# Optimization experiments

Measured on AMD Instinct MI355X. Metric: run time of the kernel, lower is better.

The kernel has to match this reference:

```python
import jax, jax.numpy as jnp
import numpy as np

N_NODES = 50000
N_EDGES = 800000
GEN_EPS = 1e-7
LN_EPS = 1e-5


def _mlp3_tanh(x, w0, b0, w1, b1, w2, b2):
    x = jnp.tanh(x @ w0.T + b0)
    x = jnp.tanh(x @ w1.T + b1)
    return jnp.tanh(x @ w2.T + b2)


def _gen_conv(x, src, dst, edge_attr, w0, b0, ln_w, ln_b, w1, b1):
    # GENConv(aggr='softmax', t=1): msg = relu(x_j + e) + eps
    msg = jax.nn.relu(x[src] + edge_attr) + GEN_EPS          # [E, 64]
    m = jax.ops.segment_max(msg, dst, num_segments=N_NODES)  # [N, 64]
    ex = jnp.exp(msg - m[dst])
    den = jax.ops.segment_sum(ex, dst, num_segments=N_NODES)
    alpha = ex / den[dst]                                    # scatter-softmax per dst
    agg = jax.ops.segment_sum(alpha * msg, dst, num_segments=N_NODES)
    h = x + agg                                              # x_r + aggregated messages
    # internal MLP: Linear(64->128), LayerNorm(128), ReLU, Linear(128->64)
    h = h @ w0.T + b0
    mu = jnp.mean(h, axis=-1, keepdims=True)
    var = jnp.mean((h - mu) ** 2, axis=-1, keepdims=True)
    h = ln_w * (h - mu) * jax.lax.rsqrt(var + LN_EPS) + ln_b
    h = jax.nn.relu(h)
    return h @ w1.T + b1


def setup_inputs() -> dict:
    key = jax.random.key(0)
    ks = jax.random.split(key, 32)
    s = 0.05
    d = {
        'node_features': jax.random.normal(ks[0], (N_NODES, 11), jnp.float32),
        'edge_features': jax.random.normal(ks[1], (N_EDGES, 3), jnp.float32),
        'edge_index': jax.random.randint(ks[2], (2, N_EDGES), 0, N_NODES, jnp.int32),
        'ne_w0': jax.random.normal(ks[3], (64, 11)) * s, 'ne_b0': jnp.zeros((64,)),
        'ne_w1': jax.random.normal(ks[4], (64, 64)) * s, 'ne_b1': jnp.zeros((64,)),
        'ne_w2': jax.random.normal(ks[5], (64, 64)) * s, 'ne_b2': jnp.zeros((64,)),
        'ee_w0': jax.random.normal(ks[6], (64, 3)) * s, 'ee_b0': jnp.zeros((64,)),
        'ee_w1': jax.random.normal(ks[7], (64, 64)) * s, 'ee_b1': jnp.zeros((64,)),
        'ee_w2': jax.random.normal(ks[8], (64, 64)) * s, 'ee_b2': jnp.zeros((64,)),
        'mp_w0': jax.random.normal(ks[9], (3, 128, 64)) * s,
        'mp_b0': jnp.zeros((3, 128)),
        'mp_ln_w': jnp.ones((3, 128)), 'mp_ln_b': jnp.zeros((3, 128)),
        'mp_w1': jax.random.normal(ks[10], (3, 64, 128)) * s,
        'mp_b1': jnp.zeros((3, 64)),
        'pi_w0': jax.random.normal(ks[11], (64, 64)) * s, 'pi_b0': jnp.zeros((64,)),
        'pi_w1': jax.random.normal(ks[12], (64, 64)) * s, 'pi_b1': jnp.zeros((64,)),
        'pi_w2': jax.random.normal(ks[13], (2, 64)) * s, 'pi_b2': jnp.zeros((2,)),
    }
    return {k: (v.astype(jnp.float32) if v.dtype != jnp.int32 else v) for k, v in d.items()}


def reference(node_features, edge_features, edge_index,
              ne_w0, ne_b0, ne_w1, ne_b1, ne_w2, ne_b2,
              ee_w0, ee_b0, ee_w1, ee_b1, ee_w2, ee_b2,
              mp_w0, mp_b0, mp_ln_w, mp_ln_b, mp_w1, mp_b1,
              pi_w0, pi_b0, pi_w1, pi_b1, pi_w2, pi_b2):
    src, dst = edge_index[0], edge_index[1]
    x = _mlp3_tanh(node_features, ne_w0, ne_b0, ne_w1, ne_b1, ne_w2, ne_b2)
    e = _mlp3_tanh(edge_features, ee_w0, ee_b0, ee_w1, ee_b1, ee_w2, ee_b2)
    for i in range(3):
        x = _gen_conv(x, src, dst, e, mp_w0[i], mp_b0[i], mp_ln_w[i], mp_ln_b[i], mp_w1[i], mp_b1[i])
    h = jnp.tanh(x @ pi_w0.T + pi_b0)
    h = jnp.tanh(h @ pi_w1.T + pi_b1)
    out = h @ pi_w2.T + pi_b2                 # [N, 2]
    # output.t().reshape(-1)[:n_turbines] == first column of out
    means = -30.0 + (out[:, 0] + 1.0) * 60.0 / 2.0
    return means
```

## Files before the change

kernel.cpp:

```cpp
#include <hip/hip_runtime.h>
#include <stdint.h>

#define N_NODES 50000
#define N_EDGES 800000

typedef unsigned short u16;
typedef unsigned int u32;
typedef __attribute__((ext_vector_type(8))) short short8;
typedef __attribute__((ext_vector_type(4))) float f32x4;
typedef __attribute__((ext_vector_type(4))) u32 u32x4;
typedef __attribute__((ext_vector_type(2))) u32 u32x2;

#define WAVE_SYNC() asm volatile("s_waitcnt lgkmcnt(0)" ::: "memory")

__device__ __forceinline__ float b2f(u16 v) {
    u32 u = ((u32)v) << 16; float f; __builtin_memcpy(&f, &u, 4); return f;
}
__device__ __forceinline__ u16 f2b(float f) {
    u32 u; __builtin_memcpy(&u, &f, 4);
    return (u16)((u + 0x8000u) >> 16);
}
__device__ __forceinline__ float lo2f(u32 p) {
    u32 u = p << 16; float f; __builtin_memcpy(&f, &u, 4); return f;
}
__device__ __forceinline__ float hi2f(u32 p) {
    u32 u = p & 0xffff0000u; float f; __builtin_memcpy(&f, &u, 4); return f;
}
__device__ __forceinline__ u32 pack2(float a, float b) {
    u32 ua, ub; __builtin_memcpy(&ua, &a, 4); __builtin_memcpy(&ub, &b, 4);
    return __builtin_amdgcn_perm(ub + 0x8000u, ua + 0x8000u, 0x07060302u);
}
__device__ __forceinline__ f32x4 mfma16(short8 a, short8 b, f32x4 c) {
    return __builtin_amdgcn_mfma_f32_16x16x32_bf16(a, b, c, 0, 0, 0);
}

#define TANH_TBL_N 192
__device__ __forceinline__ void build_tanh_tbl(float2* tbl) {
    int i = (int)threadIdx.x;
    if (i < TANH_TBL_N) {
        float x0 = i * 0.03125f, x1 = x0 + 0.03125f;
        float t0 = tanhf(x0), t1 = tanhf(x1);
        float s = (t1 - t0) * 32.f;
        tbl[i] = make_float2(fmaf(-s, x0, t0), s);
    }
    __syncthreads();
}
__device__ __forceinline__ float lut_tanh(const float2* __restrict__ tbl, float x) {
    float a = __builtin_fabsf(x);
    a = fminf(a, 5.96875f);
    int i = (int)(a * 32.f);
    float2 bs = tbl[i];
    float y = fmaf(bs.y, a, bs.x);
    u32 uy, ux; __builtin_memcpy(&uy, &y, 4); __builtin_memcpy(&ux, &x, 4);
    u32 r = (uy & 0x7fffffffu) | (ux & 0x80000000u);
    float o; __builtin_memcpy(&o, &r, 4); return o;
}

enum : int {
    NE_T0 = 0,     NE_B0 = 704,   NE_T1 = 768,   NE_B1 = 4864,  NE_T2 = 4928,  NE_B2 = 9024,
    EE_T0 = 9088,  EE_B0 = 9280,  EE_T1 = 9344,  EE_B1 = 13440, EE_T2 = 13504, EE_B2 = 17600,
    MP_T0 = 17664, MP_B0 = 42240, LNW_O = 42624, LNB_O = 43008, MP_T1 = 43392, MP_B1 = 67968,
    PI_T0 = 68160, PI_B0 = 72256, PI_T1 = 72320, PI_B1 = 76416, PI_W2 = 76480, PI_B2 = 76608,
    W_TOTAL = 76610
};

enum : int {
    FR_EE1 = 0, FR_EE2 = 4, FR_EE3 = 12, FR_NE1 = 20, FR_NE2 = 24, FR_NE3 = 32,
    FR_MP0 = 40, FR_MP1 = 88, FR_PI0 = 136, FR_PI1 = 144, FR_TOTAL = 152
};

#define OFF_W       ((size_t)0)
#define OFF_FLAG    ((size_t)0x60000)
#define OFF_WB      ((size_t)0x61000)
#define OFF_X0      ((size_t)0x90000)
#define OFF_X1      ((size_t)0x00D00000)
#define OFF_H64B    ((size_t)0x01A00000)
#define OFF_XB0     ((size_t)0x02080000)
#define OFF_E       ((size_t)0x02700000)
#define OFF_ROWPTR  ((size_t)0x08900000)
#define OFF_CURSOR  ((size_t)0x08940000)
#define OFF_PERM    ((size_t)0x08980000)
#define OFF_SRCS    ((size_t)0x08D00000)
#define OFF_BSUM    ((size_t)0x09080000)
#define OFF_XB1     ((size_t)0x09100000)

struct Ptrs24 { const void* p[24]; };


__global__ void detect_kernel(const void* nf, int* flag) {
    u32 w = ((const u32*)nf)[threadIdx.x & 63];
    u32 lo = w & 0xffffu;
    int e = (int)((lo >> 7) & 0xff);
    int good = ((e >= 118 && e <= 132) || lo == 0) ? 1 : 0;
    unsigned long long b = __ballot(good != 0);
    if (threadIdx.x == 0) *flag = (__popcll(b) >= 48) ? 1 : 0;
}

__global__ void convert_weights(Ptrs24 ps, float* __restrict__ W, const int* flag) {
    const int segIN[24] = {11,64,64,64,64,64, 3,64,64,64,64,64, 64,384,384,384,128,192, 64,64,64,64,128,2};
    const int segOUT[24]= {64, 1,64, 1,64, 1, 64, 1,64, 1,64, 1, 128, 1,  1,  1, 64,  1, 64, 1,64, 1,  1,1};
    const int segS[24]  = { 1, 1, 1, 1, 1, 1,  1, 1, 1, 1, 1, 1,   3, 1,  1,  1,  3,  1,  1, 1, 1, 1,  1,1};
    const int segTR[24] = { 1, 0, 1, 0, 1, 0,  1, 0, 1, 0, 1, 0,   1, 0,  0,  0,  1,  0,  1, 0, 1, 0,  0,0};
    int t = blockIdx.x * blockDim.x + threadIdx.x;
    if (t >= W_TOTAL) return;
    bool bf = (*flag != 0);
    int seg = 0, off = t;
    for (;;) {
        int cnt = segIN[seg] * segOUT[seg] * segS[seg];
        if (off < cnt) break;
        off -= cnt; seg++;
    }
    int srcIdx;
    if (segTR[seg]) {
        int per = segIN[seg] * segOUT[seg];
        int s = off / per, d = off % per;
        int j = d / segOUT[seg], i = d % segOUT[seg];
        srcIdx = s * per + i * segIN[seg] + j;
    } else {
        srcIdx = off;
    }
    const void* p = ps.p[seg];
    W[t] = bf ? b2f(((const u16*)p)[srcIdx]) : ((const float*)p)[srcIdx];
}

__global__ void make_frags(const float* __restrict__ W, u16* __restrict__ Wb) {
    const int base[15] = {FR_EE1,FR_EE2,FR_EE3,FR_NE1,FR_NE2,FR_NE3,
                          FR_MP0,FR_MP0+16,FR_MP0+32, FR_MP1,FR_MP1+16,FR_MP1+32,
                          FR_PI0,FR_PI1,FR_TOTAL};
    const int woff[14] = {EE_T0,EE_T1,EE_T2, NE_T0,NE_T1,NE_T2,
                          MP_T0,MP_T0+8192,MP_T0+16384, MP_T1,MP_T1+8192,MP_T1+16384,
                          PI_T0,PI_T1};
    const int kreal[14] = {3,64,64, 11,64,64, 64,64,64, 128,128,128, 64,64};
    const int nn[14]    = {64,64,64, 64,64,64, 128,128,128, 64,64,64, 64,64};
    int t = blockIdx.x * blockDim.x + threadIdx.x;
    if (t >= FR_TOTAL * 512) return;
    int f = t >> 9, r = t & 511, lane = r >> 3, j = r & 7;
    int l = 0;
    while (f >= base[l + 1]) l++;
    int lf = f - base[l];
    int NT = nn[l] >> 4;
    int kt = lf / NT, nt = lf % NT;
    int k = kt * 32 + (lane >> 4) * 8 + j;
    int n = nt * 16 + (lane & 15);
    float v = (k < kreal[l]) ? W[woff[l] + k * nn[l] + n] : 0.f;
    u32 u; __builtin_memcpy(&u, &v, 4);
    Wb[t] = (u16)((u + 0x7fffu + ((u >> 16) & 1u)) >> 16);
}


__global__ void hist_kernel(const int* __restrict__ dst, int* __restrict__ rowptr) {
    int e = blockIdx.x * blockDim.x + threadIdx.x;
    if (e < N_EDGES) atomicAdd(&rowptr[dst[e] + 1], 1);
}

__global__ void scanA(int* __restrict__ rowptr, int* __restrict__ bsum) {
    __shared__ int wsum[16];
    int tid = threadIdx.x, lane = tid & 63, wid = tid >> 6;
    int i0 = blockIdx.x * 2048 + tid * 2;
    int v0 = (i0 <= N_NODES) ? rowptr[i0] : 0;
    int v1 = (i0 + 1 <= N_NODES) ? rowptr[i0 + 1] : 0;
    int v = v0 + v1;
#pragma unroll
    for (int off = 1; off < 64; off <<= 1) {
        int t = __shfl_up(v, off, 64);
        if (lane >= off) v += t;
    }
    if (lane == 63) wsum[wid] = v;
    __syncthreads();
    if (tid == 0) { int a = 0; for (int w = 0; w < 16; w++) { a += wsum[w]; wsum[w] = a; } }
    __syncthreads();
    int incl = v + (wid ? wsum[wid - 1] : 0);
    if (i0 <= N_NODES) rowptr[i0] = incl - v1;
    if (i0 + 1 <= N_NODES) rowptr[i0 + 1] = incl;
    if (tid == 1023) bsum[blockIdx.x] = incl;
}
__global__ void scanB(int* __restrict__ bsum, int nb) {
    int lane = threadIdx.x;
    int v = (lane < nb) ? bsum[lane] : 0;
#pragma unroll
    for (int off = 1; off < 64; off <<= 1) {
        int t = __shfl_up(v, off, 64);
        if (lane >= off) v += t;
    }
    if (lane < nb) bsum[lane] = v;
}
__global__ void scanC(const int* __restrict__ bsum, int* __restrict__ rowptr,
                      int* __restrict__ cursor) {
    int i = blockIdx.x * 1024 + threadIdx.x;
    if (i > N_NODES) return;
    int b = i >> 11;
    int v = rowptr[i] + (b ? bsum[b - 1] : 0);
    rowptr[i] = v;
    if (i < N_NODES) cursor[i] = v;
}

__global__ void scatter_kernel(const int* __restrict__ dst, const int* __restrict__ src,
                               int* __restrict__ cursor, int* __restrict__ perm,
                               int* __restrict__ srcs) {
    int e = blockIdx.x * blockDim.x + threadIdx.x;
    if (e >= N_EDGES) return;
    int p = atomicAdd(&cursor[dst[e]], 1);
    perm[e] = p;
    srcs[p] = src[e];
}


template<int KT, int NT, int INSTR>
__device__ __forceinline__ void mfma_layer(const u32* ldsin, int lane,
        const short8* __restrict__ Wf, int basef, const float* __restrict__ bias, f32x4* acc) {
    int q = lane >> 4, mr = lane & 15;
#pragma unroll
    for (int nt = 0; nt < NT; nt++) acc[nt] = *(const f32x4*)(bias + nt * 16 + q * 4);
#pragma unroll
    for (int kt = 0; kt < KT; kt++) {
        short8 act = *(const short8*)(ldsin + mr * INSTR + kt * 16 + q * 4);
#pragma unroll
        for (int nt = 0; nt < NT; nt++)
            acc[nt] = mfma16(Wf[(basef + kt * NT + nt) * 64 + lane], act, acc[nt]);
    }
}

template<int KT, int NT>
__device__ __forceinline__ void mfma_layer_reg(const short8* act, int lane,
        const short8* __restrict__ Wf, int basef, const float* __restrict__ bias, f32x4* acc) {
    int q = lane >> 4;
#pragma unroll
    for (int nt = 0; nt < NT; nt++) acc[nt] = *(const f32x4*)(bias + nt * 16 + q * 4);
#pragma unroll
    for (int kt = 0; kt < KT; kt++)
#pragma unroll
        for (int nt = 0; nt < NT; nt++)
            acc[nt] = mfma16(Wf[(basef + kt * NT + nt) * 64 + lane], act[kt], acc[nt]);
}

template<int NT, int OUTSTR>
__device__ __forceinline__ void tanh_pack_lds(const f32x4* acc, u32* ldsout, int lane,
                                              const float2* __restrict__ tbl) {
    int q = lane >> 4, mr = lane & 15;
#pragma unroll
    for (int nt = 0; nt < NT; nt++) {
        f32x4 a = acc[nt];
        ldsout[mr * OUTSTR + nt * 8 + q * 2 + 0] = pack2(lut_tanh(tbl, a[0]), lut_tanh(tbl, a[1]));
        ldsout[mr * OUTSTR + nt * 8 + q * 2 + 1] = pack2(lut_tanh(tbl, a[2]), lut_tanh(tbl, a[3]));
    }
}


__global__ __launch_bounds__(256) void edge_encoder(const void* ef, u32* __restrict__ ebuf,
        const int* __restrict__ perm, const float* __restrict__ W,
        const short8* __restrict__ Wf, const int* flag) {
    __shared__ u32 lds[4 * 1152];
    __shared__ float2 tbl[TANH_TBL_N];
    build_tanh_tbl(tbl);
    int wv = threadIdx.x >> 6, lane = threadIdx.x & 63;
    u32* B0 = lds + wv * 1152;
    u32* B1 = B0 + 576;
    long ebase = (long)blockIdx.x * 64 + wv * 16;
    bool bf = (*flag != 0);
    if (lane < 16) {
        long e = ebase + lane;
        float i0, i1, i2;
        if (bf) { const u16* p = (const u16*)ef + e * 3; i0 = b2f(p[0]); i1 = b2f(p[1]); i2 = b2f(p[2]); }
        else    { const float* p = (const float*)ef + e * 3; i0 = p[0]; i1 = p[1]; i2 = p[2]; }
        u32* row = B0 + lane * 36;
        row[0] = pack2(i0, i1); row[1] = pack2(i2, 0.f);
#pragma unroll
        for (int d = 2; d < 16; d++) row[d] = 0;
    }
    WAVE_SYNC();
    f32x4 acc[4];
    mfma_layer<1, 4, 36>(B0, lane, Wf, FR_EE1, W + EE_B0, acc);
    tanh_pack_lds<4, 36>(acc, B1, lane, tbl);
    WAVE_SYNC();
    mfma_layer<2, 4, 36>(B1, lane, Wf, FR_EE2, W + EE_B1, acc);
    tanh_pack_lds<4, 36>(acc, B0, lane, tbl);
    WAVE_SYNC();
    mfma_layer<2, 4, 36>(B0, lane, Wf, FR_EE3, W + EE_B2, acc);
    tanh_pack_lds<4, 36>(acc, B1, lane, tbl);
    WAVE_SYNC();
    int ro = lane >> 2, cc = (lane & 3) * 8;
    long e = ebase + ro;
    long prow = perm[e];
    u32x4 v0 = *(const u32x4*)&B1[ro * 36 + cc];
    u32x4 v1 = *(const u32x4*)&B1[ro * 36 + cc + 4];
    *(u32x4*)&ebuf[prow * 32 + cc] = v0;
    *(u32x4*)&ebuf[prow * 32 + cc + 4] = v1;
}

__global__ __launch_bounds__(256) void node_encoder(const void* nf, float* __restrict__ x,
        u16* __restrict__ xbf, const float* __restrict__ W,
        const short8* __restrict__ Wf, const int* flag) {
    __shared__ u32 lds[4 * 1152];
    __shared__ float2 tbl[TANH_TBL_N];
    build_tanh_tbl(tbl);
    int wv = threadIdx.x >> 6, lane = threadIdx.x & 63;
    int q = lane >> 4, mr = lane & 15;
    u32* B0 = lds + wv * 1152;
    u32* B1 = B0 + 576;
    long nbase = (long)blockIdx.x * 64 + wv * 16;
    bool bf = (*flag != 0);
    if (lane < 16) {
        long n = nbase + lane;
        float in[12];
#pragma unroll
        for (int j = 0; j < 12; j++) in[j] = 0.f;
        if (n < N_NODES) {
#pragma unroll
            for (int j = 0; j < 11; j++)
                in[j] = bf ? b2f(((const u16*)nf)[n * 11 + j]) : ((const float*)nf)[n * 11 + j];
        }
        u32* row = B0 + lane * 36;
#pragma unroll
        for (int d = 0; d < 6; d++) row[d] = pack2(in[2 * d], in[2 * d + 1]);
#pragma unroll
        for (int d = 6; d < 16; d++) row[d] = 0;
    }
    WAVE_SYNC();
    f32x4 acc[4];
    mfma_layer<1, 4, 36>(B0, lane, Wf, FR_NE1, W + NE_B0, acc);
    tanh_pack_lds<4, 36>(acc, B1, lane, tbl);
    WAVE_SYNC();
    mfma_layer<2, 4, 36>(B1, lane, Wf, FR_NE2, W + NE_B1, acc);
    tanh_pack_lds<4, 36>(acc, B0, lane, tbl);
    WAVE_SYNC();
    mfma_layer<2, 4, 36>(B0, lane, Wf, FR_NE3, W + NE_B2, acc);
    long n = nbase + mr;
    if (n < N_NODES) {
#pragma unroll
        for (int nt = 0; nt < 4; nt++) {
            f32x4 v;
#pragma unroll
            for (int rr = 0; rr < 4; rr++) v[rr] = lut_tanh(tbl, acc[nt][rr]);
            *(f32x4*)(x + n * 64 + nt * 16 + q * 4) = v;
            u32x2 pb; pb.x = pack2(v[0], v[1]); pb.y = pack2(v[2], v[3]);
            *(u32x2*)&xbf[n * 64 + nt * 16 + q * 4] = pb;
        }
    }
}

__global__ __launch_bounds__(256) void aggregate_kernel(
        const float* __restrict__ x, const u32* __restrict__ xbf32,
        const u32* __restrict__ ebuf32, const int* __restrict__ srcs,
        const int* __restrict__ rowptr, u32* __restrict__ h64bf32) {
    int gw = (int)((blockIdx.x * 256 + threadIdx.x) >> 6);
    int lane = (int)(threadIdx.x & 63);
    if (gw >= N_NODES) return;
    gw = __builtin_amdgcn_readfirstlane(gw);
    int half = lane >> 5, h = lane & 31;
    int beg = rowptr[gw], end = rowptr[gw + 1];
    int cnt = end - beg;
    float num0 = 0.f, den0 = 0.f, num1 = 0.f, den1 = 0.f;
    for (int base = 0; base < cnt; base += 64) {
        int rem = cnt - base; if (rem > 64) rem = 64;
        int lidx = (lane < rem) ? lane : (rem - 1);
        int sk = srcs[beg + base + lidx];
        const u32* eb = ebuf32 + (long)(beg + base) * 32 + h;
        int iters = (rem + 1) >> 1;
#pragma unroll 2
        for (int t = 0; t < iters; t++) {
            int eo = 2 * t + half;
            int eoc = (eo < rem) ? eo : (rem - 1);
            int s = __shfl(sk, eo, 64);
            u32 xv = xbf32[(long)s * 32 + h];
            u32 ev = eb[eoc * 32];
            float m0 = fmaxf(lo2f(xv) + lo2f(ev), 0.f) + 1e-7f;
            float m1 = fmaxf(hi2f(xv) + hi2f(ev), 0.f) + 1e-7f;
            bool act = eo < rem;
            float w0 = act ? __expf(m0) : 0.f;
            float w1 = act ? __expf(m1) : 0.f;
            num0 = fmaf(w0, m0, num0); den0 += w0;
            num1 = fmaf(w1, m1, num1); den1 += w1;
        }
    }
    num0 += __shfl_xor(num0, 32, 64); den0 += __shfl_xor(den0, 32, 64);
    num1 += __shfl_xor(num1, 32, 64); den1 += __shfl_xor(den1, 32, 64);
    if (half == 0) {
        float agg0 = (den0 > 0.f) ? __fdividef(num0, den0) : 0.f;
        float agg1 = (den1 > 0.f) ? __fdividef(num1, den1) : 0.f;
        float2 xr = *(const float2*)(x + (long)gw * 64 + 2 * h);
        h64bf32[(long)gw * 32 + h] = pack2(xr.x + agg0, xr.y + agg1);
    }
}

__global__ __launch_bounds__(256) void mlp_fused(const u16* __restrict__ h64bf,
        float* __restrict__ xout, u16* __restrict__ xbf,
        const float* __restrict__ W, const short8* __restrict__ Wf, int r) {
    __shared__ u32 lds[4 * 1088];
    int wv = threadIdx.x >> 6, lane = threadIdx.x & 63;
    int q = lane >> 4, mr = lane & 15;
    u32* bufY = lds + wv * 1088;
    long nbase = (long)blockIdx.x * 64 + wv * 16;
    long row = nbase + mr;
    long rc = (row < N_NODES) ? row : (N_NODES - 1);
    short8 act[2];
#pragma unroll
    for (int kt = 0; kt < 2; kt++)
        act[kt] = *(const short8*)&h64bf[rc * 64 + kt * 32 + q * 8];
    f32x4 acc[8];
    mfma_layer_reg<2, 8>(act, lane, Wf, FR_MP0 + r * 16, W + MP_B0 + r * 128, acc);
    float s = 0.f, sq = 0.f;
#pragma unroll
    for (int nt = 0; nt < 8; nt++)
#pragma unroll
        for (int rr = 0; rr < 4; rr++) { float v = acc[nt][rr]; s += v; sq = fmaf(v, v, sq); }
    s += __shfl_xor(s, 16, 64);  s += __shfl_xor(s, 32, 64);
    sq += __shfl_xor(sq, 16, 64); sq += __shfl_xor(sq, 32, 64);
    float mu = s * (1.f / 128.f);
    float var = sq * (1.f / 128.f) - mu * mu;
    float inv = rsqrtf(var + 1e-5f);
    const float* LW = W + LNW_O + r * 128;
    const float* LB = W + LNB_O + r * 128;
#pragma unroll
    for (int nt = 0; nt < 8; nt++) {
        f32x4 lw = *(const f32x4*)(LW + nt * 16 + q * 4);
        f32x4 lb = *(const f32x4*)(LB + nt * 16 + q * 4);
        float u0 = fmaxf(fmaf((acc[nt][0] - mu) * inv, lw[0], lb[0]), 0.f);
        float u1 = fmaxf(fmaf((acc[nt][1] - mu) * inv, lw[1], lb[1]), 0.f);
        float u2 = fmaxf(fmaf((acc[nt][2] - mu) * inv, lw[2], lb[2]), 0.f);
        float u3 = fmaxf(fmaf((acc[nt][3] - mu) * inv, lw[3], lb[3]), 0.f);
        bufY[mr * 68 + nt * 8 + q * 2 + 0] = pack2(u0, u1);
        bufY[mr * 68 + nt * 8 + q * 2 + 1] = pack2(u2, u3);
    }
    WAVE_SYNC();
    f32x4 acc2[4];
    mfma_layer<4, 4, 68>(bufY, lane, Wf, FR_MP1 + r * 16, W + MP_B1 + r * 64, acc2);
    if (row < N_NODES) {
#pragma unroll
        for (int nt = 0; nt < 4; nt++) {
            f32x4 v = acc2[nt];
            *(f32x4*)(xout + row * 64 + nt * 16 + q * 4) = v;
            u32x2 pb; pb.x = pack2(v[0], v[1]); pb.y = pack2(v[2], v[3]);
            *(u32x2*)&xbf[row * 64 + nt * 16 + q * 4] = pb;
        }
    }
}

__global__ __launch_bounds__(256) void policy_head(const u16* __restrict__ xbf, void* out,
        const float* __restrict__ W, const short8* __restrict__ Wf, const int* flag) {
    __shared__ u32 lds[4 * 576];
    __shared__ float2 tbl[TANH_TBL_N];
    build_tanh_tbl(tbl);
    int wv = threadIdx.x >> 6, lane = threadIdx.x & 63;
    int q = lane >> 4, mr = lane & 15;
    u32* bufY = lds + wv * 576;
    long nbase = (long)blockIdx.x * 64 + wv * 16;
    long row = nbase + mr;
    long rc = (row < N_NODES) ? row : (N_NODES - 1);
    bool bf = (*flag != 0);
    short8 act[2];
#pragma unroll
    for (int kt = 0; kt < 2; kt++)
        act[kt] = *(const short8*)&xbf[rc * 64 + kt * 32 + q * 8];
    f32x4 acc[4];
    mfma_layer_reg<2, 4>(act, lane, Wf, FR_PI0, W + PI_B0, acc);
    tanh_pack_lds<4, 36>(acc, bufY, lane, tbl);
    WAVE_SYNC();
    mfma_layer<2, 4, 36>(bufY, lane, Wf, FR_PI1, W + PI_B1, acc);
    float o = 0.f;
#pragma unroll
    for (int nt = 0; nt < 4; nt++) {
        f32x4 w2 = *(const f32x4*)(W + PI_W2 + nt * 16 + q * 4);
#pragma unroll
        for (int rr = 0; rr < 4; rr++) o = fmaf(lut_tanh(tbl, acc[nt][rr]), w2[rr], o);
    }
    o += __shfl_xor(o, 16, 64);
    o += __shfl_xor(o, 32, 64);
    if (lane < 16 && row < N_NODES) {
        float means = 30.f * (o + W[PI_B2]);
        if (bf) ((u16*)out)[row] = f2b(means);
        else    ((float*)out)[row] = means;
    }
}

extern "C" void kernel_launch(void* const* d_in, const int* in_sizes, int n_in,
                              void* d_out, int out_size, void* d_ws, size_t ws_size,
                              hipStream_t stream) {
    char* ws = (char*)d_ws;
    float* W      = (float*)(ws + OFF_W);
    int*   flag   = (int*)(ws + OFF_FLAG);
    u16*   Wb     = (u16*)(ws + OFF_WB);
    const short8* Wf = (const short8*)(ws + OFF_WB);
    float* x0     = (float*)(ws + OFF_X0);
    float* x1     = (float*)(ws + OFF_X1);
    u16*   xb0    = (u16*)(ws + OFF_XB0);
    u16*   xb1    = (u16*)(ws + OFF_XB1);
    u16*   h64bf  = (u16*)(ws + OFF_H64B);
    u32*   h64b32 = (u32*)(ws + OFF_H64B);
    u32*   ebuf32 = (u32*)(ws + OFF_E);
    int*   rowptr = (int*)(ws + OFF_ROWPTR);
    int*   cursor = (int*)(ws + OFF_CURSOR);
    int*   perm   = (int*)(ws + OFF_PERM);
    int*   srcs   = (int*)(ws + OFF_SRCS);
    int*   bsum   = (int*)(ws + OFF_BSUM);

    const int* ei   = (const int*)d_in[2];
    const int* srcv = ei;
    const int* dstv = ei + N_EDGES;

    detect_kernel<<<1, 64, 0, stream>>>(d_in[0], flag);
    hipMemsetAsync(rowptr, 0, (N_NODES + 1) * sizeof(int), stream);

    Ptrs24 ps;
    for (int k = 0; k < 24; k++) ps.p[k] = d_in[3 + k];
    convert_weights<<<(W_TOTAL + 255) / 256, 256, 0, stream>>>(ps, W, flag);
    make_frags<<<(FR_TOTAL * 512 + 255) / 256, 256, 0, stream>>>(W, Wb);

    hist_kernel<<<(N_EDGES + 255) / 256, 256, 0, stream>>>(dstv, rowptr);
    scanA<<<25, 1024, 0, stream>>>(rowptr, bsum);
    scanB<<<1, 64, 0, stream>>>(bsum, 25);
    scanC<<<(N_NODES + 1024) / 1024, 1024, 0, stream>>>(bsum, rowptr, cursor);
    scatter_kernel<<<(N_EDGES + 255) / 256, 256, 0, stream>>>(dstv, srcv, cursor, perm, srcs);

    node_encoder<<<(N_NODES + 63) / 64, 256, 0, stream>>>(d_in[0], x0, xb0, W, Wf, flag);
    edge_encoder<<<N_EDGES / 64, 256, 0, stream>>>(d_in[1], ebuf32, perm, W, Wf, flag);

    float* xc = x0; float* xn = x1;
    u16* xbc = xb0; u16* xbn = xb1;
    for (int r = 0; r < 3; r++) {
        aggregate_kernel<<<(N_NODES * 64 + 255) / 256, 256, 0, stream>>>(
            xc, (const u32*)xbc, ebuf32, srcs, rowptr, h64b32);
        mlp_fused<<<(N_NODES + 63) / 64, 256, 0, stream>>>(h64bf, xn, xbn, W, Wf, r);
        float* t = xc; xc = xn; xn = t;
        u16* tb = xbc; xbc = xbn; xbn = tb;
    }
    policy_head<<<(N_NODES + 63) / 64, 256, 0, stream>>>(xbc, d_out, W, Wf, flag);
}
```

Baseline: 463.6 us.

## Pad CSR segments to even length, process four nodes per wave, drop fp32 x

The CSR row layout now rounds each node's edge count up to an even number, with padding slots marked by srcs=-1 (memset 0xFF). This lets the aggregate loop handle edge pairs without per-iteration bounds clamping. Each wave now aggregates four consecutive nodes and reuses a sliding window of source indices loaded once per 64 edges. The fp32 copies of the node features are removed, so the residual x is read from bf16, which cuts memory traffic but lowers precision of the skip connection. Padding edges read ebuf entries that were never written, but their contribution is masked by the validity check.

```diff
diff --git a/kernel.cpp b/kernel.cpp
--- a/kernel.cpp
+++ b/kernel.cpp
@@ -51,9 +51,7 @@
     int i = (int)(a * 32.f);
     float2 bs = tbl[i];
     float y = fmaf(bs.y, a, bs.x);
-    u32 uy, ux; __builtin_memcpy(&uy, &y, 4); __builtin_memcpy(&ux, &x, 4);
-    u32 r = (uy & 0x7fffffffu) | (ux & 0x80000000u);
-    float o; __builtin_memcpy(&o, &r, 4); return o;
+    return copysignf(y, x);
 }
 
 enum : int {
@@ -72,17 +70,16 @@
 #define OFF_W       ((size_t)0)
 #define OFF_FLAG    ((size_t)0x60000)
 #define OFF_WB      ((size_t)0x61000)
-#define OFF_X0      ((size_t)0x90000)
-#define OFF_X1      ((size_t)0x00D00000)
-#define OFF_H64B    ((size_t)0x01A00000)
-#define OFF_XB0     ((size_t)0x02080000)
-#define OFF_E       ((size_t)0x02700000)
-#define OFF_ROWPTR  ((size_t)0x08900000)
-#define OFF_CURSOR  ((size_t)0x08940000)
-#define OFF_PERM    ((size_t)0x08980000)
-#define OFF_SRCS    ((size_t)0x08D00000)
-#define OFF_BSUM    ((size_t)0x09080000)
-#define OFF_XB1     ((size_t)0x09100000)
+#define OFF_XB0     ((size_t)0x90000)
+#define OFF_XB1     ((size_t)0x700000)
+#define OFF_H64B    ((size_t)0xE00000)
+#define OFF_E       ((size_t)0x1500000)
+#define OFF_ROWPTR  ((size_t)0x8300000)
+#define OFF_CURSOR  ((size_t)0x8340000)
+#define OFF_CNT     ((size_t)0x8380000)
+#define OFF_PERM    ((size_t)0x83C0000)
+#define OFF_SRCS    ((size_t)0x8700000)
+#define OFF_BSUM    ((size_t)0x8A80000)
 
 struct Ptrs24 { const void* p[24]; };
 
@@ -148,17 +145,19 @@
 }
 
 
-__global__ void hist_kernel(const int* __restrict__ dst, int* __restrict__ rowptr) {
+__global__ void hist_kernel(const int* __restrict__ dst, int* __restrict__ cnts) {
     int e = blockIdx.x * blockDim.x + threadIdx.x;
-    if (e < N_EDGES) atomicAdd(&rowptr[dst[e] + 1], 1);
-}
-
-__global__ void scanA(int* __restrict__ rowptr, int* __restrict__ bsum) {
+    if (e < N_EDGES) atomicAdd(&cnts[dst[e]], 1);
+}
+
+__global__ void scanA(const int* __restrict__ cnts, int* __restrict__ prow,
+                      int* __restrict__ bsum) {
     __shared__ int wsum[16];
     int tid = threadIdx.x, lane = tid & 63, wid = tid >> 6;
     int i0 = blockIdx.x * 2048 + tid * 2;
-    int v0 = (i0 <= N_NODES) ? rowptr[i0] : 0;
-    int v1 = (i0 + 1 <= N_NODES) ? rowptr[i0 + 1] : 0;
+    int v0 = 0, v1 = 0;
+    if (i0 >= 1 && i0 <= N_NODES) v0 = (cnts[i0 - 1] + 1) & ~1;
+    if (i0 + 1 <= N_NODES && i0 + 1 >= 1) v1 = (cnts[i0] + 1) & ~1;
     int v = v0 + v1;
 #pragma unroll
     for (int off = 1; off < 64; off <<= 1) {
@@ -170,8 +169,8 @@
     if (tid == 0) { int a = 0; for (int w = 0; w < 16; w++) { a += wsum[w]; wsum[w] = a; } }
     __syncthreads();
     int incl = v + (wid ? wsum[wid - 1] : 0);
-    if (i0 <= N_NODES) rowptr[i0] = incl - v1;
-    if (i0 + 1 <= N_NODES) rowptr[i0 + 1] = incl;
+    if (i0 <= N_NODES) prow[i0] = incl - v1;
+    if (i0 + 1 <= N_NODES) prow[i0 + 1] = incl;
     if (tid == 1023) bsum[blockIdx.x] = incl;
 }
 __global__ void scanB(int* __restrict__ bsum, int nb) {
@@ -184,13 +183,13 @@
     }
     if (lane < nb) bsum[lane] = v;
 }
-__global__ void scanC(const int* __restrict__ bsum, int* __restrict__ rowptr,
+__global__ void scanC(const int* __restrict__ bsum, int* __restrict__ prow,
                       int* __restrict__ cursor) {
     int i = blockIdx.x * 1024 + threadIdx.x;
     if (i > N_NODES) return;
     int b = i >> 11;
-    int v = rowptr[i] + (b ? bsum[b - 1] : 0);
-    rowptr[i] = v;
+    int v = prow[i] + (b ? bsum[b - 1] : 0);
+    prow[i] = v;
     if (i < N_NODES) cursor[i] = v;
 }
 
@@ -280,14 +279,14 @@
     WAVE_SYNC();
     int ro = lane >> 2, cc = (lane & 3) * 8;
     long e = ebase + ro;
-    long prow = perm[e];
+    long prowp = perm[e];
     u32x4 v0 = *(const u32x4*)&B1[ro * 36 + cc];
     u32x4 v1 = *(const u32x4*)&B1[ro * 36 + cc + 4];
-    *(u32x4*)&ebuf[prow * 32 + cc] = v0;
-    *(u32x4*)&ebuf[prow * 32 + cc + 4] = v1;
-}
-
-__global__ __launch_bounds__(256) void node_encoder(const void* nf, float* __restrict__ x,
+    *(u32x4*)&ebuf[prowp * 32 + cc] = v0;
+    *(u32x4*)&ebuf[prowp * 32 + cc + 4] = v1;
+}
+
+__global__ __launch_bounds__(256) void node_encoder(const void* nf,
         u16* __restrict__ xbf, const float* __restrict__ W,
         const short8* __restrict__ Wf, const int* flag) {
     __shared__ u32 lds[4 * 1152];
@@ -328,62 +327,61 @@
     if (n < N_NODES) {
 #pragma unroll
         for (int nt = 0; nt < 4; nt++) {
-            f32x4 v;
-#pragma unroll
-            for (int rr = 0; rr < 4; rr++) v[rr] = lut_tanh(tbl, acc[nt][rr]);
-            *(f32x4*)(x + n * 64 + nt * 16 + q * 4) = v;
-            u32x2 pb; pb.x = pack2(v[0], v[1]); pb.y = pack2(v[2], v[3]);
+            float v0 = lut_tanh(tbl, acc[nt][0]), v1 = lut_tanh(tbl, acc[nt][1]);
+            float v2 = lut_tanh(tbl, acc[nt][2]), v3 = lut_tanh(tbl, acc[nt][3]);
+            u32x2 pb; pb.x = pack2(v0, v1); pb.y = pack2(v2, v3);
             *(u32x2*)&xbf[n * 64 + nt * 16 + q * 4] = pb;
         }
     }
 }
 
 __global__ __launch_bounds__(256) void aggregate_kernel(
-        const float* __restrict__ x, const u32* __restrict__ xbf32,
-        const u32* __restrict__ ebuf32, const int* __restrict__ srcs,
-        const int* __restrict__ rowptr, u32* __restrict__ h64bf32) {
-    int gw = (int)((blockIdx.x * 256 + threadIdx.x) >> 6);
+        const u32* __restrict__ xbf32, const u32* __restrict__ ebuf32,
+        const int* __restrict__ srcs, const int* __restrict__ prow,
+        u32* __restrict__ h64bf32) {
+    int wid = (int)((blockIdx.x * 256 + threadIdx.x) >> 6);
     int lane = (int)(threadIdx.x & 63);
-    if (gw >= N_NODES) return;
-    gw = __builtin_amdgcn_readfirstlane(gw);
+    int n0 = __builtin_amdgcn_readfirstlane(wid) * 4;
+    if (n0 >= N_NODES) return;
     int half = lane >> 5, h = lane & 31;
-    int beg = rowptr[gw], end = rowptr[gw + 1];
-    int cnt = end - beg;
-    float num0 = 0.f, den0 = 0.f, num1 = 0.f, den1 = 0.f;
-    for (int base = 0; base < cnt; base += 64) {
-        int rem = cnt - base; if (rem > 64) rem = 64;
-        int lidx = (lane < rem) ? lane : (rem - 1);
-        int sk = srcs[beg + base + lidx];
-        const u32* eb = ebuf32 + (long)(beg + base) * 32 + h;
-        int iters = (rem + 1) >> 1;
-#pragma unroll 2
-        for (int t = 0; t < iters; t++) {
-            int eo = 2 * t + half;
-            int eoc = (eo < rem) ? eo : (rem - 1);
-            int s = __shfl(sk, eo, 64);
-            u32 xv = xbf32[(long)s * 32 + h];
-            u32 ev = eb[eoc * 32];
+    int rl = n0 + (lane < 4 ? lane : 4);
+    if (rl > N_NODES) rl = N_NODES;
+    int rv = prow[rl];
+    int win = __shfl(rv, 0, 64);
+    int sk = srcs[win + lane];
+    for (int j = 0; j < 4; j++) {
+        int n = n0 + j;
+        if (n >= N_NODES) break;
+        int kb = __shfl(rv, j, 64);
+        int ke = __shfl(rv, j + 1, 64);
+        u32 xr = xbf32[(long)n * 32 + h];
+        float num0 = 0.f, den0 = 0.f, num1 = 0.f, den1 = 0.f;
+        for (int k = kb; k < ke; k += 2) {
+            if (k + 1 >= win + 64) { win = k; sk = srcs[win + lane]; }
+            int s = __shfl(sk, k - win + half, 64);
+            u32 ev = ebuf32[(long)(k + half) * 32 + h];
+            bool valid = s >= 0;
+            long sr = valid ? (long)s : 0;
+            u32 xv = xbf32[sr * 32 + h];
             float m0 = fmaxf(lo2f(xv) + lo2f(ev), 0.f) + 1e-7f;
             float m1 = fmaxf(hi2f(xv) + hi2f(ev), 0.f) + 1e-7f;
-            bool act = eo < rem;
-            float w0 = act ? __expf(m0) : 0.f;
-            float w1 = act ? __expf(m1) : 0.f;
+            float w0 = valid ? __expf(m0) : 0.f;
+            float w1 = valid ? __expf(m1) : 0.f;
             num0 = fmaf(w0, m0, num0); den0 += w0;
             num1 = fmaf(w1, m1, num1); den1 += w1;
         }
-    }
-    num0 += __shfl_xor(num0, 32, 64); den0 += __shfl_xor(den0, 32, 64);
-    num1 += __shfl_xor(num1, 32, 64); den1 += __shfl_xor(den1, 32, 64);
-    if (half == 0) {
-        float agg0 = (den0 > 0.f) ? __fdividef(num0, den0) : 0.f;
-        float agg1 = (den1 > 0.f) ? __fdividef(num1, den1) : 0.f;
-        float2 xr = *(const float2*)(x + (long)gw * 64 + 2 * h);
-        h64bf32[(long)gw * 32 + h] = pack2(xr.x + agg0, xr.y + agg1);
+        num0 += __shfl_xor(num0, 32, 64); den0 += __shfl_xor(den0, 32, 64);
+        num1 += __shfl_xor(num1, 32, 64); den1 += __shfl_xor(den1, 32, 64);
+        if (half == 0) {
+            float agg0 = (den0 > 0.f) ? __fdividef(num0, den0) : 0.f;
+            float agg1 = (den1 > 0.f) ? __fdividef(num1, den1) : 0.f;
+            h64bf32[(long)n * 32 + h] = pack2(lo2f(xr) + agg0, hi2f(xr) + agg1);
+        }
     }
 }
 
 __global__ __launch_bounds__(256) void mlp_fused(const u16* __restrict__ h64bf,
-        float* __restrict__ xout, u16* __restrict__ xbf,
+        u16* __restrict__ xbf,
         const float* __restrict__ W, const short8* __restrict__ Wf, int r) {
     __shared__ u32 lds[4 * 1088];
     int wv = threadIdx.x >> 6, lane = threadIdx.x & 63;
@@ -428,7 +426,6 @@
 #pragma unroll
         for (int nt = 0; nt < 4; nt++) {
             f32x4 v = acc2[nt];
-            *(f32x4*)(xout + row * 64 + nt * 16 + q * 4) = v;
             u32x2 pb; pb.x = pack2(v[0], v[1]); pb.y = pack2(v[2], v[3]);
             *(u32x2*)&xbf[row * 64 + nt * 16 + q * 4] = pb;
         }
@@ -480,15 +477,14 @@
     int*   flag   = (int*)(ws + OFF_FLAG);
     u16*   Wb     = (u16*)(ws + OFF_WB);
     const short8* Wf = (const short8*)(ws + OFF_WB);
-    float* x0     = (float*)(ws + OFF_X0);
-    float* x1     = (float*)(ws + OFF_X1);
     u16*   xb0    = (u16*)(ws + OFF_XB0);
     u16*   xb1    = (u16*)(ws + OFF_XB1);
     u16*   h64bf  = (u16*)(ws + OFF_H64B);
     u32*   h64b32 = (u32*)(ws + OFF_H64B);
     u32*   ebuf32 = (u32*)(ws + OFF_E);
-    int*   rowptr = (int*)(ws + OFF_ROWPTR);
+    int*   prow   = (int*)(ws + OFF_ROWPTR);
     int*   cursor = (int*)(ws + OFF_CURSOR);
+    int*   cnts   = (int*)(ws + OFF_CNT);
     int*   perm   = (int*)(ws + OFF_PERM);
     int*   srcs   = (int*)(ws + OFF_SRCS);
     int*   bsum   = (int*)(ws + OFF_BSUM);
@@ -498,29 +494,29 @@
     const int* dstv = ei + N_EDGES;
 
     detect_kernel<<<1, 64, 0, stream>>>(d_in[0], flag);
-    hipMemsetAsync(rowptr, 0, (N_NODES + 1) * sizeof(int), stream);
+    hipMemsetAsync(cnts, 0, N_NODES * sizeof(int), stream);
+    hipMemsetAsync(srcs, 0xFF, (size_t)0x340000, stream);
 
     Ptrs24 ps;
     for (int k = 0; k < 24; k++) ps.p[k] = d_in[3 + k];
     convert_weights<<<(W_TOTAL + 255) / 256, 256, 0, stream>>>(ps, W, flag);
     make_frags<<<(FR_TOTAL * 512 + 255) / 256, 256, 0, stream>>>(W, Wb);
 
-    hist_kernel<<<(N_EDGES + 255) / 256, 256, 0, stream>>>(dstv, rowptr);
-    scanA<<<25, 1024, 0, stream>>>(rowptr, bsum);
+    hist_kernel<<<(N_EDGES + 255) / 256, 256, 0, stream>>>(dstv, cnts);
+    scanA<<<25, 1024, 0, stream>>>(cnts, prow, bsum);
     scanB<<<1, 64, 0, stream>>>(bsum, 25);
-    scanC<<<(N_NODES + 1024) / 1024, 1024, 0, stream>>>(bsum, rowptr, cursor);
+    scanC<<<(N_NODES + 1024) / 1024, 1024, 0, stream>>>(bsum, prow, cursor);
     scatter_kernel<<<(N_EDGES + 255) / 256, 256, 0, stream>>>(dstv, srcv, cursor, perm, srcs);
 
-    node_encoder<<<(N_NODES + 63) / 64, 256, 0, stream>>>(d_in[0], x0, xb0, W, Wf, flag);
+    node_encoder<<<(N_NODES + 63) / 64, 256, 0, stream>>>(d_in[0], xb0, W, Wf, flag);
     edge_encoder<<<N_EDGES / 64, 256, 0, stream>>>(d_in[1], ebuf32, perm, W, Wf, flag);
 
-    float* xc = x0; float* xn = x1;
     u16* xbc = xb0; u16* xbn = xb1;
+    const int aggBlocks = ((N_NODES + 3) / 4 * 64 + 255) / 256;
     for (int r = 0; r < 3; r++) {
-        aggregate_kernel<<<(N_NODES * 64 + 255) / 256, 256, 0, stream>>>(
-            xc, (const u32*)xbc, ebuf32, srcs, rowptr, h64b32);
-        mlp_fused<<<(N_NODES + 63) / 64, 256, 0, stream>>>(h64bf, xn, xbn, W, Wf, r);
-        float* t = xc; xc = xn; xn = t;
+        aggregate_kernel<<<aggBlocks, 256, 0, stream>>>(
+            (const u32*)xbc, ebuf32, srcs, prow, h64b32);
+        mlp_fused<<<(N_NODES + 63) / 64, 256, 0, stream>>>(h64bf, xbn, W, Wf, r);
         u16* tb = xbc; xbc = xbn; xbn = tb;
     }
     policy_head<<<(N_NODES + 63) / 64, 256, 0, stream>>>(xbc, d_out, W, Wf, flag);
```

After: 461.9 us. No clear change (-0.4%).
